# Performance work log

Measured on AMD Instinct MI355X. Metric: run time of the kernel, lower is better.

Reference implementation:

```python
import jax, jax.numpy as jnp
import numpy as np

N_STATE = 1024
N_HEAD = 16
B = 2
S = 2048


def setup_inputs() -> dict:
    key = jax.random.key(0)
    ks = jax.random.split(key, 8)
    s = 0.02
    x = jax.random.normal(ks[0], (B, S, N_STATE), dtype=jnp.float32)
    # causal additive mask, as in Whisper: upper triangle = -inf
    mask = jnp.where(jnp.triu(jnp.ones((S, S), dtype=bool), k=1), -jnp.inf, 0.0).astype(jnp.float32)
    Wq = jax.random.normal(ks[1], (N_STATE, N_STATE), dtype=jnp.float32) * s
    bq = jax.random.normal(ks[2], (N_STATE,), dtype=jnp.float32) * s
    Wk = jax.random.normal(ks[3], (N_STATE, N_STATE), dtype=jnp.float32) * s
    Wv = jax.random.normal(ks[4], (N_STATE, N_STATE), dtype=jnp.float32) * s
    bv = jax.random.normal(ks[5], (N_STATE,), dtype=jnp.float32) * s
    Wo = jax.random.normal(ks[6], (N_STATE, N_STATE), dtype=jnp.float32) * s
    bo = jax.random.normal(ks[7], (N_STATE,), dtype=jnp.float32) * s
    return {"x": x, "mask": mask, "Wq": Wq, "bq": bq, "Wk": Wk,
            "Wv": Wv, "bv": bv, "Wo": Wo, "bo": bo}


def reference(x, mask, Wq, bq, Wk, Wv, bv, Wo, bo):
    Bb, S_, D = x.shape
    H = N_HEAD
    hd = D // H
    scale = hd ** (-0.25)  # scale split across q and k, as in the source
    q = x @ Wq.T + bq              # [B,S,D]
    k = x @ Wk.T                   # key has no bias
    v = x @ Wv.T + bv
    # [B,S,D] -> [B,H,S,hd]
    q = q.reshape(Bb, S_, H, hd).transpose(0, 2, 1, 3) * scale
    k = k.reshape(Bb, S_, H, hd).transpose(0, 2, 1, 3) * scale
    v = v.reshape(Bb, S_, H, hd).transpose(0, 2, 1, 3)
    qk = jnp.einsum('bhsd,bhtd->bhst', q, k) + mask[:S_, :S_]
    w = jax.nn.softmax(qk, axis=-1).astype(q.dtype)
    out = jnp.einsum('bhst,bhtd->bhsd', w, v)
    out = out.transpose(0, 2, 1, 3).reshape(Bb, S_, D)
    return out @ Wo.T + bo
```

## Files before the change

### kernel.cpp

```cpp
#include <hip/hip_runtime.h>
#include <hip/hip_bf16.h>
#include <cmath>

typedef __bf16 bf16;
typedef __bf16 bf16x8 __attribute__((ext_vector_type(8)));
typedef __bf16 bf16x4 __attribute__((ext_vector_type(4)));
typedef float f32x4 __attribute__((ext_vector_type(4)));

__device__ __forceinline__ void load16_to_lds(const void* g, void* l) {
    __builtin_amdgcn_global_load_lds(
        (const __attribute__((address_space(1))) unsigned int*)g,
        (__attribute__((address_space(3))) unsigned int*)l, 16, 0, 0);
}

__global__ __launch_bounds__(256) void convert_kernel(
    const float* __restrict__ x,  const float* __restrict__ wq,
    const float* __restrict__ wk, const float* __restrict__ wv,
    const float* __restrict__ wo, bf16* __restrict__ dst)
{
    const size_t M1 = 1024ull * 1024ull, M4 = 4ull * M1;
    size_t i0 = ((size_t)blockIdx.x * 256 + threadIdx.x) * 8;
    const float* s;
    size_t off;
    if      (i0 < M4)        { s = x;  off = i0; }
    else if (i0 < M4 + M1)   { s = wq; off = i0 - M4; }
    else if (i0 < M4 + 2*M1) { s = wk; off = i0 - M4 - M1; }
    else if (i0 < M4 + 3*M1) { s = wv; off = i0 - M4 - 2*M1; }
    else                     { s = wo; off = i0 - M4 - 3*M1; }
    float4 a = *(const float4*)(s + off);
    float4 b = *(const float4*)(s + off + 4);
    bf16x8 r = { (bf16)a.x, (bf16)a.y, (bf16)a.z, (bf16)a.w,
                 (bf16)b.x, (bf16)b.y, (bf16)b.z, (bf16)b.w };
    *(bf16x8*)(dst + i0) = r;
}

template<int BM, bool OUT_F32>
__device__ __forceinline__ void gemm_core(
    const bf16* __restrict__ A, const bf16* __restrict__ W,
    const float* __restrict__ bias, void* __restrict__ C,
    int mb, int nb, bool vt_out)
{
    constexpr int IF = BM / 32;
    __shared__ __align__(16) bf16 As[BM * 64];
    __shared__ __align__(16) bf16 Bs[128 * 64];

    const int tid  = threadIdx.x;
    const int lane = tid & 63;
    const int wave = tid >> 6;
    const int wr   = (wave >> 1) * (BM / 2);
    const int wc   = (wave & 1) * 64;
    const int l15  = lane & 15;
    const int l4   = lane >> 4;

    f32x4 acc[IF][4] = {};

    for (int kt = 0; kt < 16; ++kt) {
#pragma unroll
        for (int it = 0; it < BM / 32; ++it) {
            int c = it * 256 + tid;
            load16_to_lds(&A[(size_t)(mb * BM + (c >> 3)) * 1024 + kt * 64 + (c & 7) * 8],
                          &As[(it * 256 + (tid & 192)) * 8]);
        }
#pragma unroll
        for (int it = 0; it < 4; ++it) {
            int c = it * 256 + tid;
            load16_to_lds(&W[(size_t)(nb * 128 + (c >> 3)) * 1024 + kt * 64 + (c & 7) * 8],
                          &Bs[(it * 256 + (tid & 192)) * 8]);
        }
        __syncthreads();
#pragma unroll
        for (int kk = 0; kk < 2; ++kk) {
            bf16x8 af[IF], bfr[4];
#pragma unroll
            for (int i = 0; i < IF; ++i)
                af[i] = *(const bf16x8*)&As[(wr + i * 16 + l15) * 64 + kk * 32 + l4 * 8];
#pragma unroll
            for (int j = 0; j < 4; ++j)
                bfr[j] = *(const bf16x8*)&Bs[(wc + j * 16 + l15) * 64 + kk * 32 + l4 * 8];
#pragma unroll
            for (int i = 0; i < IF; ++i)
#pragma unroll
                for (int j = 0; j < 4; ++j)
                    acc[i][j] = __builtin_amdgcn_mfma_f32_16x16x32_bf16(
                        af[i], bfr[j], acc[i][j], 0, 0, 0);
        }
        __syncthreads();
    }

    if (!OUT_F32 && vt_out) {
#pragma unroll
        for (int j = 0; j < 4; ++j) {
            int col = nb * 128 + wc + j * 16 + l15;
            float bv = bias ? bias[col] : 0.f;
            int h = col >> 6, d = col & 63;
#pragma unroll
            for (int i = 0; i < IF; ++i) {
                int m0 = mb * BM + wr + i * 16 + l4 * 4;
                int b = m0 >> 11, s = m0 & 2047;
                bf16x4 pk = { (bf16)(acc[i][j][0] + bv), (bf16)(acc[i][j][1] + bv),
                              (bf16)(acc[i][j][2] + bv), (bf16)(acc[i][j][3] + bv) };
                *(bf16x4*)&((bf16*)C)[(size_t)((b * 16 + h) * 64 + d) * 2048 + s] = pk;
            }
        }
    } else {
#pragma unroll
        for (int j = 0; j < 4; ++j) {
            int col = nb * 128 + wc + j * 16 + l15;
            float bv = bias ? bias[col] : 0.f;
#pragma unroll
            for (int i = 0; i < IF; ++i) {
                int row0 = mb * BM + wr + i * 16 + l4 * 4;
#pragma unroll
                for (int r = 0; r < 4; ++r) {
                    float val = acc[i][j][r] + bv;
                    size_t idx = (size_t)(row0 + r) * 1024 + col;
                    if (OUT_F32) ((float*)C)[idx] = val;
                    else         ((bf16*)C)[idx]  = (bf16)val;
                }
            }
        }
    }
}

__global__ __launch_bounds__(256) void qkv_kernel(
    const bf16* __restrict__ xb,
    const bf16* __restrict__ wqb, const float* __restrict__ bq,
    const bf16* __restrict__ wkb,
    const bf16* __restrict__ wvb, const float* __restrict__ bv,
    bf16* __restrict__ q, bf16* __restrict__ k, bf16* __restrict__ vt)
{
    int mb = blockIdx.x;
    int nbg = blockIdx.y;
    int sel = nbg >> 3, nb = nbg & 7;
    const bf16* W = (sel == 0) ? wqb : ((sel == 1) ? wkb : wvb);
    const float* bias = (sel == 0) ? bq : ((sel == 2) ? bv : nullptr);
    bf16* C = (sel == 0) ? q : ((sel == 1) ? k : vt);
    gemm_core<128, false>(xb, W, bias, C, mb, nb, sel == 2);
}

__global__ __launch_bounds__(256) void oproj_kernel(
    const bf16* __restrict__ ao, const bf16* __restrict__ wob,
    const float* __restrict__ bo, float* __restrict__ out)
{
    gemm_core<64, true>(ao, wob, bo, out, blockIdx.x, blockIdx.y, false);
}

__global__ __launch_bounds__(256) void attn_kernel(
    const bf16* __restrict__ q, const bf16* __restrict__ k,
    const bf16* __restrict__ vt, bf16* __restrict__ o)
{
    __shared__ __align__(16) bf16 Ks[2][64 * 64];
    __shared__ __align__(16) bf16 Vs[2][64 * 64];
    __shared__ __align__(16) bf16 Ps[4][16 * 72];

    const int tid  = threadIdx.x;
    const int lane = tid & 63;
    const int wave = tid >> 6;
    const int l15  = lane & 15;
    const int l4   = lane >> 4;

    const int pairIdx = blockIdx.x;
    const int bh = blockIdx.y;
    const int b = bh >> 4, h = bh & 15;
    const int qts[2] = { pairIdx, 31 - pairIdx };

    auto stage = [&](int nt, int buf) {
#pragma unroll
        for (int it = 0; it < 2; ++it) {
            int c = it * 256 + tid;
            load16_to_lds(&k[(size_t)(b * 2048 + nt * 64 + (c >> 3)) * 1024 + h * 64 + (c & 7) * 8],
                          &Ks[buf][(it * 256 + (tid & 192)) * 8]);
            load16_to_lds(&vt[(size_t)(bh * 64 + (c >> 3)) * 2048 + nt * 64 + (c & 7) * 8],
                          &Vs[buf][(it * 256 + (tid & 192)) * 8]);
        }
    };

    int b0 = 0;
    stage(0, 0);

    const float QS = 0.18033688f;

    for (int seg = 0; seg < 2; ++seg) {
        const int qt = qts[seg];
        const int qg = qt * 64 + wave * 16 + l15;
        bf16x8 qf[2];
#pragma unroll
        for (int kk = 0; kk < 2; ++kk) {
            bf16x8 t = *(const bf16x8*)&q[(size_t)(b * 2048 + qg) * 1024 + h * 64 + kk * 32 + l4 * 8];
#pragma unroll
            for (int e = 0; e < 8; ++e) qf[kk][e] = (bf16)((float)t[e] * QS);
        }

        f32x4 oacc[4] = {};
        float lsum = 0.f;

        const int n = qt + 1;
        for (int nt = 0; nt < n; ++nt) {
            __syncthreads();
            if (nt + 1 < n)      stage(nt + 1, b0 ^ 1);
            else if (seg == 0)   stage(qts[1] ? 0 : 0, b0 ^ 1);

            f32x4 s[4] = {};
#pragma unroll
            for (int kk = 0; kk < 2; ++kk) {
                bf16x8 qk = qf[kk];
#pragma unroll
                for (int j = 0; j < 4; ++j) {
                    bf16x8 kf = *(const bf16x8*)&Ks[b0][(j * 16 + l15) * 64 + kk * 32 + l4 * 8];
                    s[j] = __builtin_amdgcn_mfma_f32_16x16x32_bf16(kf, qk, s[j], 0, 0, 0);
                }
            }

            float pv[4][4];
            if (nt == qt) {
#pragma unroll
                for (int j = 0; j < 4; ++j)
#pragma unroll
                    for (int r = 0; r < 4; ++r) {
                        int kg = nt * 64 + j * 16 + l4 * 4 + r;
                        pv[j][r] = (kg > qg) ? 0.f
                                 : __builtin_amdgcn_exp2f(s[j][r]);
                    }
            } else {
#pragma unroll
                for (int j = 0; j < 4; ++j)
#pragma unroll
                    for (int r = 0; r < 4; ++r)
                        pv[j][r] = __builtin_amdgcn_exp2f(s[j][r]);
            }
#pragma unroll
            for (int j = 0; j < 4; ++j)
                lsum += (pv[j][0] + pv[j][1]) + (pv[j][2] + pv[j][3]);

#pragma unroll
            for (int j = 0; j < 4; ++j) {
                bf16x4 pk = { (bf16)pv[j][0], (bf16)pv[j][1], (bf16)pv[j][2], (bf16)pv[j][3] };
                *(bf16x4*)&Ps[wave][l15 * 72 + j * 16 + l4 * 4] = pk;
            }

#pragma unroll
            for (int kk = 0; kk < 2; ++kk) {
                bf16x8 pf = *(const bf16x8*)&Ps[wave][l15 * 72 + kk * 32 + l4 * 8];
#pragma unroll
                for (int f = 0; f < 4; ++f) {
                    bf16x8 vf = *(const bf16x8*)&Vs[b0][(f * 16 + l15) * 64 + kk * 32 + l4 * 8];
                    oacc[f] = __builtin_amdgcn_mfma_f32_16x16x32_bf16(pf, vf, oacc[f], 0, 0, 0);
                }
            }
            b0 ^= 1;
        }

        lsum += __shfl_xor(lsum, 16, 64);
        lsum += __shfl_xor(lsum, 32, 64);
        float rinv[4];
#pragma unroll
        for (int r = 0; r < 4; ++r) rinv[r] = 1.f / __shfl(lsum, l4 * 4 + r, 64);
#pragma unroll
        for (int f = 0; f < 4; ++f)
#pragma unroll
            for (int r = 0; r < 4; ++r)
                o[(size_t)(b * 2048 + qt * 64 + wave * 16 + l4 * 4 + r) * 1024 + h * 64 + f * 16 + l15]
                    = (bf16)(oacc[f][r] * rinv[r]);
    }
}

extern "C" void kernel_launch(void* const* d_in, const int* in_sizes, int n_in,
                              void* d_out, int out_size, void* d_ws, size_t ws_size,
                              hipStream_t stream)
{
    const float* x  = (const float*)d_in[0];
    const float* Wq = (const float*)d_in[2];
    const float* bq = (const float*)d_in[3];
    const float* Wk = (const float*)d_in[4];
    const float* Wv = (const float*)d_in[5];
    const float* bv = (const float*)d_in[6];
    const float* Wo = (const float*)d_in[7];
    const float* bo = (const float*)d_in[8];
    float* out = (float*)d_out;

    const size_t M1 = 1024ull * 1024ull, M4 = 4ull * M1;
    bf16* base = (bf16*)d_ws;
    bf16* xb  = base;
    bf16* wqb = base + M4;
    bf16* wkb = base + M4 + M1;
    bf16* wvb = base + M4 + 2 * M1;
    bf16* wob = base + M4 + 3 * M1;
    bf16* q   = base + 8 * M1;
    bf16* k   = base + 12 * M1;
    bf16* vt  = base + 16 * M1;
    bf16* ao  = xb;

    convert_kernel<<<4096, 256, 0, stream>>>(x, Wq, Wk, Wv, Wo, base);
    qkv_kernel<<<dim3(32, 24), 256, 0, stream>>>(xb, wqb, bq, wkb, wvb, bv, q, k, vt);
    attn_kernel<<<dim3(16, 32), 256, 0, stream>>>(q, k, vt, ao);
    oproj_kernel<<<dim3(64, 8), 256, 0, stream>>>(ao, wob, bo, out);
}
```

Measured before the change: 224.1 us.

## Swizzle LDS tiles, fold Q scale into weights, one q-tile per attention block

The GEMM core now uses a K-tile of 32 with an XOR-swizzled LDS layout, and the attention K/V tiles are also XOR-swizzled. Both changes aim to remove LDS bank conflicts on the bf16x8 fragment reads. The softmax Q scale is folded into the Wq conversion and the bq bias, so the per-element rescale inside attention goes away. Attention now launches one query tile per block (1024 blocks) instead of pairing tiles for load balance, with the longest tiles scheduled first. The trade-off is twice as many GEMM K iterations and barriers, and less even work per attention block.

After: 217.8 us. -2.8%, faster.

```diff
diff --git a/kernel.cpp b/kernel.cpp
--- a/kernel.cpp
+++ b/kernel.cpp
@@ -7,6 +7,8 @@
 typedef __bf16 bf16x4 __attribute__((ext_vector_type(4)));
 typedef float f32x4 __attribute__((ext_vector_type(4)));
 
+#define QS 0.18033688f
+
 __device__ __forceinline__ void load16_to_lds(const void* g, void* l) {
     __builtin_amdgcn_global_load_lds(
         (const __attribute__((address_space(1))) unsigned int*)g,
@@ -22,15 +24,16 @@
     size_t i0 = ((size_t)blockIdx.x * 256 + threadIdx.x) * 8;
     const float* s;
     size_t off;
+    float sc = 1.f;
     if      (i0 < M4)        { s = x;  off = i0; }
-    else if (i0 < M4 + M1)   { s = wq; off = i0 - M4; }
+    else if (i0 < M4 + M1)   { s = wq; off = i0 - M4; sc = QS; }
     else if (i0 < M4 + 2*M1) { s = wk; off = i0 - M4 - M1; }
     else if (i0 < M4 + 3*M1) { s = wv; off = i0 - M4 - 2*M1; }
     else                     { s = wo; off = i0 - M4 - 3*M1; }
     float4 a = *(const float4*)(s + off);
     float4 b = *(const float4*)(s + off + 4);
-    bf16x8 r = { (bf16)a.x, (bf16)a.y, (bf16)a.z, (bf16)a.w,
-                 (bf16)b.x, (bf16)b.y, (bf16)b.z, (bf16)b.w };
+    bf16x8 r = { (bf16)(a.x*sc), (bf16)(a.y*sc), (bf16)(a.z*sc), (bf16)(a.w*sc),
+                 (bf16)(b.x*sc), (bf16)(b.y*sc), (bf16)(b.z*sc), (bf16)(b.w*sc) };
     *(bf16x8*)(dst + i0) = r;
 }
 
@@ -38,11 +41,11 @@
 __device__ __forceinline__ void gemm_core(
     const bf16* __restrict__ A, const bf16* __restrict__ W,
     const float* __restrict__ bias, void* __restrict__ C,
-    int mb, int nb, bool vt_out)
+    int mb, int nb, bool vt_out, float bias_scale)
 {
     constexpr int IF = BM / 32;
-    __shared__ __align__(16) bf16 As[BM * 64];
-    __shared__ __align__(16) bf16 Bs[128 * 64];
+    __shared__ __align__(16) bf16 As[BM * 32];
+    __shared__ __align__(16) bf16 Bs[128 * 32];
 
     const int tid  = threadIdx.x;
     const int lane = tid & 63;
@@ -51,39 +54,39 @@
     const int wc   = (wave & 1) * 64;
     const int l15  = lane & 15;
     const int l4   = lane >> 4;
+    const int swz  = (l4 ^ ((l15 >> 1) & 3)) * 8;
 
     f32x4 acc[IF][4] = {};
 
-    for (int kt = 0; kt < 16; ++kt) {
-#pragma unroll
-        for (int it = 0; it < BM / 32; ++it) {
+    for (int kt = 0; kt < 32; ++kt) {
+#pragma unroll
+        for (int it = 0; it < BM / 64; ++it) {
             int c = it * 256 + tid;
-            load16_to_lds(&A[(size_t)(mb * BM + (c >> 3)) * 1024 + kt * 64 + (c & 7) * 8],
+            int scol = ((c & 3) ^ ((c >> 3) & 3)) * 8;
+            load16_to_lds(&A[(size_t)(mb * BM + (c >> 2)) * 1024 + kt * 32 + scol],
                           &As[(it * 256 + (tid & 192)) * 8]);
         }
 #pragma unroll
-        for (int it = 0; it < 4; ++it) {
+        for (int it = 0; it < 2; ++it) {
             int c = it * 256 + tid;
-            load16_to_lds(&W[(size_t)(nb * 128 + (c >> 3)) * 1024 + kt * 64 + (c & 7) * 8],
+            int scol = ((c & 3) ^ ((c >> 3) & 3)) * 8;
+            load16_to_lds(&W[(size_t)(nb * 128 + (c >> 2)) * 1024 + kt * 32 + scol],
                           &Bs[(it * 256 + (tid & 192)) * 8]);
         }
         __syncthreads();
-#pragma unroll
-        for (int kk = 0; kk < 2; ++kk) {
-            bf16x8 af[IF], bfr[4];
-#pragma unroll
-            for (int i = 0; i < IF; ++i)
-                af[i] = *(const bf16x8*)&As[(wr + i * 16 + l15) * 64 + kk * 32 + l4 * 8];
+        bf16x8 af[IF], bfr[4];
+#pragma unroll
+        for (int i = 0; i < IF; ++i)
+            af[i] = *(const bf16x8*)&As[(wr + i * 16 + l15) * 32 + swz];
+#pragma unroll
+        for (int j = 0; j < 4; ++j)
+            bfr[j] = *(const bf16x8*)&Bs[(wc + j * 16 + l15) * 32 + swz];
+#pragma unroll
+        for (int i = 0; i < IF; ++i)
 #pragma unroll
             for (int j = 0; j < 4; ++j)
-                bfr[j] = *(const bf16x8*)&Bs[(wc + j * 16 + l15) * 64 + kk * 32 + l4 * 8];
-#pragma unroll
-            for (int i = 0; i < IF; ++i)
-#pragma unroll
-                for (int j = 0; j < 4; ++j)
-                    acc[i][j] = __builtin_amdgcn_mfma_f32_16x16x32_bf16(
-                        af[i], bfr[j], acc[i][j], 0, 0, 0);
-        }
+                acc[i][j] = __builtin_amdgcn_mfma_f32_16x16x32_bf16(
+                    af[i], bfr[j], acc[i][j], 0, 0, 0);
         __syncthreads();
     }
 
@@ -106,7 +109,7 @@
 #pragma unroll
         for (int j = 0; j < 4; ++j) {
             int col = nb * 128 + wc + j * 16 + l15;
-            float bv = bias ? bias[col] : 0.f;
+            float bv = bias ? bias[col] * bias_scale : 0.f;
 #pragma unroll
             for (int i = 0; i < IF; ++i) {
                 int row0 = mb * BM + wr + i * 16 + l4 * 4;
@@ -135,14 +138,15 @@
     const bf16* W = (sel == 0) ? wqb : ((sel == 1) ? wkb : wvb);
     const float* bias = (sel == 0) ? bq : ((sel == 2) ? bv : nullptr);
     bf16* C = (sel == 0) ? q : ((sel == 1) ? k : vt);
-    gemm_core<128, false>(xb, W, bias, C, mb, nb, sel == 2);
+    gemm_core<128, false>(xb, W, bias, C, mb, nb, sel == 2,
+                          sel == 0 ? QS : 1.f);
 }
 
 __global__ __launch_bounds__(256) void oproj_kernel(
     const bf16* __restrict__ ao, const bf16* __restrict__ wob,
     const float* __restrict__ bo, float* __restrict__ out)
 {
-    gemm_core<64, true>(ao, wob, bo, out, blockIdx.x, blockIdx.y, false);
+    gemm_core<64, true>(ao, wob, bo, out, blockIdx.x, blockIdx.y, false, 1.f);
 }
 
 __global__ __launch_bounds__(256) void attn_kernel(
@@ -159,109 +163,98 @@
     const int l15  = lane & 15;
     const int l4   = lane >> 4;
 
-    const int pairIdx = blockIdx.x;
+    const int qt = 31 - blockIdx.x;
     const int bh = blockIdx.y;
     const int b = bh >> 4, h = bh & 15;
-    const int qts[2] = { pairIdx, 31 - pairIdx };
 
     auto stage = [&](int nt, int buf) {
 #pragma unroll
         for (int it = 0; it < 2; ++it) {
             int c = it * 256 + tid;
-            load16_to_lds(&k[(size_t)(b * 2048 + nt * 64 + (c >> 3)) * 1024 + h * 64 + (c & 7) * 8],
+            int scol = ((c & 7) ^ ((c >> 3) & 7)) * 8;
+            load16_to_lds(&k[(size_t)(b * 2048 + nt * 64 + (c >> 3)) * 1024 + h * 64 + scol],
                           &Ks[buf][(it * 256 + (tid & 192)) * 8]);
-            load16_to_lds(&vt[(size_t)(bh * 64 + (c >> 3)) * 2048 + nt * 64 + (c & 7) * 8],
+            load16_to_lds(&vt[(size_t)(bh * 64 + (c >> 3)) * 2048 + nt * 64 + scol],
                           &Vs[buf][(it * 256 + (tid & 192)) * 8]);
         }
     };
 
+    const int qg = qt * 64 + wave * 16 + l15;
+    bf16x8 qf[2];
+#pragma unroll
+    for (int kk = 0; kk < 2; ++kk)
+        qf[kk] = *(const bf16x8*)&q[(size_t)(b * 2048 + qg) * 1024 + h * 64 + kk * 32 + l4 * 8];
+
+    f32x4 oacc[4] = {};
+    float lsum = 0.f;
     int b0 = 0;
     stage(0, 0);
 
-    const float QS = 0.18033688f;
-
-    for (int seg = 0; seg < 2; ++seg) {
-        const int qt = qts[seg];
-        const int qg = qt * 64 + wave * 16 + l15;
-        bf16x8 qf[2];
+    for (int nt = 0; nt <= qt; ++nt) {
+        __syncthreads();
+        if (nt < qt) stage(nt + 1, b0 ^ 1);
+
+        f32x4 s[4] = {};
 #pragma unroll
         for (int kk = 0; kk < 2; ++kk) {
-            bf16x8 t = *(const bf16x8*)&q[(size_t)(b * 2048 + qg) * 1024 + h * 64 + kk * 32 + l4 * 8];
-#pragma unroll
-            for (int e = 0; e < 8; ++e) qf[kk][e] = (bf16)((float)t[e] * QS);
-        }
-
-        f32x4 oacc[4] = {};
-        float lsum = 0.f;
-
-        const int n = qt + 1;
-        for (int nt = 0; nt < n; ++nt) {
-            __syncthreads();
-            if (nt + 1 < n)      stage(nt + 1, b0 ^ 1);
-            else if (seg == 0)   stage(qts[1] ? 0 : 0, b0 ^ 1);
-
-            f32x4 s[4] = {};
-#pragma unroll
-            for (int kk = 0; kk < 2; ++kk) {
-                bf16x8 qk = qf[kk];
-#pragma unroll
-                for (int j = 0; j < 4; ++j) {
-                    bf16x8 kf = *(const bf16x8*)&Ks[b0][(j * 16 + l15) * 64 + kk * 32 + l4 * 8];
-                    s[j] = __builtin_amdgcn_mfma_f32_16x16x32_bf16(kf, qk, s[j], 0, 0, 0);
+#pragma unroll
+            for (int j = 0; j < 4; ++j) {
+                bf16x8 kf = *(const bf16x8*)&Ks[b0][(j * 16 + l15) * 64
+                                + (((kk * 4 + l4) ^ (l15 & 7)) * 8)];
+                s[j] = __builtin_amdgcn_mfma_f32_16x16x32_bf16(kf, qf[kk], s[j], 0, 0, 0);
+            }
+        }
+
+        float pv[4][4];
+        if (nt == qt) {
+#pragma unroll
+            for (int j = 0; j < 4; ++j)
+#pragma unroll
+                for (int r = 0; r < 4; ++r) {
+                    int kg = nt * 64 + j * 16 + l4 * 4 + r;
+                    pv[j][r] = (kg > qg) ? 0.f : __builtin_amdgcn_exp2f(s[j][r]);
                 }
-            }
-
-            float pv[4][4];
-            if (nt == qt) {
-#pragma unroll
-                for (int j = 0; j < 4; ++j)
-#pragma unroll
-                    for (int r = 0; r < 4; ++r) {
-                        int kg = nt * 64 + j * 16 + l4 * 4 + r;
-                        pv[j][r] = (kg > qg) ? 0.f
-                                 : __builtin_amdgcn_exp2f(s[j][r]);
-                    }
-            } else {
-#pragma unroll
-                for (int j = 0; j < 4; ++j)
-#pragma unroll
-                    for (int r = 0; r < 4; ++r)
-                        pv[j][r] = __builtin_amdgcn_exp2f(s[j][r]);
-            }
+        } else {
 #pragma unroll
             for (int j = 0; j < 4; ++j)
-                lsum += (pv[j][0] + pv[j][1]) + (pv[j][2] + pv[j][3]);
-
-#pragma unroll
-            for (int j = 0; j < 4; ++j) {
-                bf16x4 pk = { (bf16)pv[j][0], (bf16)pv[j][1], (bf16)pv[j][2], (bf16)pv[j][3] };
-                *(bf16x4*)&Ps[wave][l15 * 72 + j * 16 + l4 * 4] = pk;
-            }
-
-#pragma unroll
-            for (int kk = 0; kk < 2; ++kk) {
-                bf16x8 pf = *(const bf16x8*)&Ps[wave][l15 * 72 + kk * 32 + l4 * 8];
-#pragma unroll
-                for (int f = 0; f < 4; ++f) {
-                    bf16x8 vf = *(const bf16x8*)&Vs[b0][(f * 16 + l15) * 64 + kk * 32 + l4 * 8];
-                    oacc[f] = __builtin_amdgcn_mfma_f32_16x16x32_bf16(pf, vf, oacc[f], 0, 0, 0);
-                }
-            }
-            b0 ^= 1;
-        }
-
-        lsum += __shfl_xor(lsum, 16, 64);
-        lsum += __shfl_xor(lsum, 32, 64);
-        float rinv[4];
-#pragma unroll
-        for (int r = 0; r < 4; ++r) rinv[r] = 1.f / __shfl(lsum, l4 * 4 + r, 64);
-#pragma unroll
-        for (int f = 0; f < 4; ++f)
-#pragma unroll
-            for (int r = 0; r < 4; ++r)
-                o[(size_t)(b * 2048 + qt * 64 + wave * 16 + l4 * 4 + r) * 1024 + h * 64 + f * 16 + l15]
-                    = (bf16)(oacc[f][r] * rinv[r]);
+#pragma unroll
+                for (int r = 0; r < 4; ++r)
+                    pv[j][r] = __builtin_amdgcn_exp2f(s[j][r]);
+        }
+#pragma unroll
+        for (int j = 0; j < 4; ++j)
+            lsum += (pv[j][0] + pv[j][1]) + (pv[j][2] + pv[j][3]);
+
+#pragma unroll
+        for (int j = 0; j < 4; ++j) {
+            bf16x4 pk = { (bf16)pv[j][0], (bf16)pv[j][1], (bf16)pv[j][2], (bf16)pv[j][3] };
+            *(bf16x4*)&Ps[wave][l15 * 72 + j * 16 + l4 * 4] = pk;
+        }
+
+#pragma unroll
+        for (int kk = 0; kk < 2; ++kk) {
+            bf16x8 pf = *(const bf16x8*)&Ps[wave][l15 * 72 + kk * 32 + l4 * 8];
+#pragma unroll
+            for (int f = 0; f < 4; ++f) {
+                bf16x8 vf = *(const bf16x8*)&Vs[b0][(f * 16 + l15) * 64
+                                + (((kk * 4 + l4) ^ (l15 & 7)) * 8)];
+                oacc[f] = __builtin_amdgcn_mfma_f32_16x16x32_bf16(pf, vf, oacc[f], 0, 0, 0);
+            }
+        }
+        b0 ^= 1;
     }
+
+    lsum += __shfl_xor(lsum, 16, 64);
+    lsum += __shfl_xor(lsum, 32, 64);
+    float rinv[4];
+#pragma unroll
+    for (int r = 0; r < 4; ++r) rinv[r] = 1.f / __shfl(lsum, l4 * 4 + r, 64);
+#pragma unroll
+    for (int f = 0; f < 4; ++f)
+#pragma unroll
+        for (int r = 0; r < 4; ++r)
+            o[(size_t)(b * 2048 + qt * 64 + wave * 16 + l4 * 4 + r) * 1024 + h * 64 + f * 16 + l15]
+                = (bf16)(oacc[f][r] * rinv[r]);
 }
 
 extern "C" void kernel_launch(void* const* d_in, const int* in_sizes, int n_in,
@@ -292,6 +285,6 @@
 
     convert_kernel<<<4096, 256, 0, stream>>>(x, Wq, Wk, Wv, Wo, base);
     qkv_kernel<<<dim3(32, 24), 256, 0, stream>>>(xb, wqb, bq, wkb, wvb, bv, q, k, vt);
-    attn_kernel<<<dim3(16, 32), 256, 0, stream>>>(q, k, vt, ao);
+    attn_kernel<<<dim3(32, 32), 256, 0, stream>>>(q, k, vt, ao);
     oproj_kernel<<<dim3(64, 8), 256, 0, stream>>>(ao, wob, bo, out);
 }
```
